# Performance work log

Hardware: AMD Instinct MI355X
Metric: run time of the kernel (lower is better)

The kernel has to match this reference:

```python
import jax, jax.numpy as jnp
import numpy as np

NUM_HEADS = 16


def setup_inputs() -> dict:
    key = jax.random.key(0)
    ks = jax.random.split(key, 9)
    B, N, D = 2, 2048, 1024
    w = 0.02
    return {
        "x": jax.random.normal(ks[0], (B, N, D), dtype=jnp.float32),
        "wq": jax.random.normal(ks[1], (D, D), dtype=jnp.float32) * w,
        "bq": jax.random.normal(ks[2], (D,), dtype=jnp.float32) * w,
        "wk": jax.random.normal(ks[3], (D, D), dtype=jnp.float32) * w,
        "bk": jax.random.normal(ks[4], (D,), dtype=jnp.float32) * w,
        "wv": jax.random.normal(ks[5], (D, D), dtype=jnp.float32) * w,
        "bv": jax.random.normal(ks[6], (D,), dtype=jnp.float32) * w,
        "wo": jax.random.normal(ks[7], (D, D), dtype=jnp.float32) * w,
        "bo": jax.random.normal(ks[8], (D,), dtype=jnp.float32) * w,
    }


def _heads(t, B, N, H, hd):
    # (B, N, D) -> (B, H, N, hd)
    return t.reshape(B, N, H, hd).transpose(0, 2, 1, 3)


def reference(x, wq, bq, wk, bk, wv, bv, wo, bo):
    B, N, D = x.shape
    H = NUM_HEADS
    hd = D // H
    q = _heads(x @ wq.T + bq, B, N, H, hd)
    k = _heads(x @ wk.T + bk, B, N, H, hd)
    v = _heads(x @ wv.T + bv, B, N, H, hd)
    # pairwise L2 distances via GEMM expansion: ||q-k||^2 = |q|^2 + |k|^2 - 2 q.k
    q2 = jnp.sum(q * q, axis=-1)                      # (B, H, N)
    k2 = jnp.sum(k * k, axis=-1)                      # (B, H, N)
    qk = jnp.einsum('bhid,bhjd->bhij', q, k)          # (B, H, N, N)
    d2 = jnp.maximum(q2[..., :, None] + k2[..., None, :] - 2.0 * qk, 1e-12)
    attn = jax.nn.softmax(-jnp.sqrt(d2), axis=-1)     # (B, H, N, N)
    out = jnp.einsum('bhij,bhjd->bhid', attn, v)      # (B, H, N, hd)
    out = out.transpose(0, 2, 1, 3).reshape(B, N, D)
    return out @ wo.T + bo
```

## Files before the change

### kernel.cpp

```cpp
#include <hip/hip_runtime.h>


typedef __attribute__((ext_vector_type(8))) short sh8;
typedef __attribute__((ext_vector_type(4))) short sh4;
typedef __attribute__((ext_vector_type(4))) float f4;

#define QK_SCALE 1.44269504f
#define D2_CLAMP 2.0814e-12f

__device__ __forceinline__ float bf2f(short s) {
  union { unsigned u; float f; } c;
  c.u = ((unsigned)(unsigned short)s) << 16;
  return c.f;
}
__device__ __forceinline__ short f2bf(float f) {
  union { float f; unsigned u; } c;
  c.f = f;
  return (short)((c.u + 0x8000u) >> 16);
}
__device__ __forceinline__ sh8 pack8(f4 a, f4 b) {
  sh8 r;
  r[0] = f2bf(a[0]); r[1] = f2bf(a[1]); r[2] = f2bf(a[2]); r[3] = f2bf(a[3]);
  r[4] = f2bf(b[0]); r[5] = f2bf(b[1]); r[6] = f2bf(b[2]); r[7] = f2bf(b[3]);
  return r;
}
__device__ __forceinline__ float exp2neg(float x) {
  return __builtin_amdgcn_exp2f(-x);
}

#define GLDS16(g, l)                                                      \
  __builtin_amdgcn_global_load_lds(                                       \
      (__attribute__((address_space(1))) void*)(void*)(g),                \
      (__attribute__((address_space(3))) void*)(void*)(l), 16, 0, 0)

__global__ __launch_bounds__(256) void cvt_bf16(const float* __restrict__ src,
                                                short* __restrict__ dst, int n) {
  const int i = (blockIdx.x * 256 + threadIdx.x) * 8;
  if (i < n)
    *(sh8*)(dst + i) = pack8(*(const f4*)(src + i), *(const f4*)(src + i + 4));
}

__global__ __launch_bounds__(256) void cvt_w4(
    const float* __restrict__ wq, const float* __restrict__ wk,
    const float* __restrict__ wv, const float* __restrict__ wo,
    short* __restrict__ dst) {
  const float* srcs[4] = {wq, wk, wv, wo};
  const float* s = srcs[blockIdx.y];
  short* d = dst + (size_t)blockIdx.y * 1048576;
  const int i = (blockIdx.x * 256 + threadIdx.x) * 8;
  *(sh8*)(d + i) = pack8(*(const f4*)(s + i), *(const f4*)(s + i + 4));
}

__global__ __launch_bounds__(256) void gemm_qkvp(
    const float* __restrict__ X, const float* __restrict__ Wq,
    const float* __restrict__ Bq, const float* __restrict__ Wk,
    const float* __restrict__ Bk, const float* __restrict__ Wv,
    const float* __restrict__ Bv, short* __restrict__ Qp,
    short* __restrict__ Kp, short* __restrict__ Vtp, int w0, int nblkP) {
  __shared__ short As[128 * 32];
  __shared__ short Bs[128 * 32];
  const int t = threadIdx.x;
  const int wave = t >> 6;
  const int lane = t & 63;
  const int l15 = lane & 15;
  const int quad = lane >> 4;
  const int m0 = blockIdx.y * 128;
  const int which = blockIdx.x / nblkP;
  const int n0l = (blockIdx.x % nblkP) * 128;
  const int wrow0 = w0 + n0l;
  const float* W = (which == 0) ? Wq : ((which == 1) ? Wk : Wv);
  const float* Bias = (which == 0) ? Bq : ((which == 1) ? Bk : Bv);
  const float qkscl = (which == 2) ? 1.0f : QK_SCALE;
  const int wm = (wave & 1) * 64;
  const int wn = (wave >> 1) * 64;

  f4 acc[4][4];
#pragma unroll
  for (int i = 0; i < 4; ++i)
#pragma unroll
    for (int j = 0; j < 4; ++j) acc[i][j] = (f4){0.f, 0.f, 0.f, 0.f};

  const float* ag = X + (size_t)(m0 + (t >> 2)) * 1024 + (t & 3) * 8;
  const float* bg = W + (size_t)(wrow0 + (t >> 2)) * 1024 + (t & 3) * 8;

  for (int kt = 0; kt < 1024; kt += 32) {
    const sh8 a0 = pack8(*(const f4*)(ag + kt), *(const f4*)(ag + kt + 4));
    const sh8 a1 =
        pack8(*(const f4*)(ag + 65536 + kt), *(const f4*)(ag + 65536 + kt + 4));
    const sh8 b0 = pack8(*(const f4*)(bg + kt), *(const f4*)(bg + kt + 4));
    const sh8 b1 =
        pack8(*(const f4*)(bg + 65536 + kt), *(const f4*)(bg + 65536 + kt + 4));
    __syncthreads();
    *(sh8*)(As + t * 8) = a0;
    *(sh8*)(As + 2048 + t * 8) = a1;
    *(sh8*)(Bs + t * 8) = b0;
    *(sh8*)(Bs + 2048 + t * 8) = b1;
    __syncthreads();
    sh8 af[4], bf[4];
#pragma unroll
    for (int i = 0; i < 4; ++i) {
      af[i] = *(const sh8*)(As + (wm + i * 16 + l15) * 32 + quad * 8);
      bf[i] = *(const sh8*)(Bs + (wn + i * 16 + l15) * 32 + quad * 8);
    }
#pragma unroll
    for (int i = 0; i < 4; ++i)
#pragma unroll
      for (int j = 0; j < 4; ++j)
        acc[i][j] =
            __builtin_amdgcn_mfma_f32_16x16x32_bf16(af[i], bf[j], acc[i][j], 0, 0, 0);
  }

#pragma unroll
  for (int j = 0; j < 4; ++j) {
    const int ngl = n0l + wn + j * 16 + l15;
    const float bias = Bias[w0 + ngl];
    const int hl = ngl >> 6;
    const int d = ngl & 63;
#pragma unroll
    for (int i = 0; i < 4; ++i) {
#pragma unroll
      for (int r = 0; r < 4; ++r) {
        const int m = m0 + wm + i * 16 + quad * 4 + r;
        const int slot = (m >> 11) * 16 + hl;
        const int mm = m & 2047;
        const short o = f2bf((acc[i][j][r] + bias) * qkscl);
        if (which == 0)
          Qp[((size_t)slot * 2048 + mm) * 64 + d] = o;
        else if (which == 1)
          Kp[((size_t)slot * 2048 + mm) * 64 + d] = o;
        else
          Vtp[((size_t)slot * 64 + d) * 2048 + mm] = o;
      }
    }
  }
}

__global__ __launch_bounds__(256) void gemm_qkv_bf(
    const short* __restrict__ X, const short* __restrict__ Wq,
    const float* __restrict__ Bq, const short* __restrict__ Wk,
    const float* __restrict__ Bk, const short* __restrict__ Wv,
    const float* __restrict__ Bv, short* __restrict__ Qp,
    short* __restrict__ Kp, short* __restrict__ Vtp) {
  __shared__ short As[128 * 32];
  __shared__ short Bs[128 * 32];
  const int t = threadIdx.x;
  const int wave = t >> 6;
  const int lane = t & 63;
  const int l15 = lane & 15;
  const int quad = lane >> 4;
  const int m0 = blockIdx.y * 128;
  const int which = blockIdx.x >> 3;
  const int n0l = (blockIdx.x & 7) * 128;
  const short* W = (which == 0) ? Wq : ((which == 1) ? Wk : Wv);
  const float* Bias = (which == 0) ? Bq : ((which == 1) ? Bk : Bv);
  const float qkscl = (which == 2) ? 1.0f : QK_SCALE;
  const int wm = (wave & 1) * 64;
  const int wn = (wave >> 1) * 64;

  f4 acc[4][4];
#pragma unroll
  for (int i = 0; i < 4; ++i)
#pragma unroll
    for (int j = 0; j < 4; ++j) acc[i][j] = (f4){0.f, 0.f, 0.f, 0.f};

  const short* ag = X + (size_t)(m0 + (t >> 2)) * 1024 + (t & 3) * 8;
  const short* bg = W + (size_t)(n0l + (t >> 2)) * 1024 + (t & 3) * 8;
  short* al = As + wave * 512;
  short* bl = Bs + wave * 512;

  for (int kt = 0; kt < 1024; kt += 32) {
    __syncthreads();
    GLDS16(ag + kt, al);
    GLDS16(ag + 65536 + kt, al + 2048);
    GLDS16(bg + kt, bl);
    GLDS16(bg + 65536 + kt, bl + 2048);
    __syncthreads();
    sh8 af[4], bf[4];
#pragma unroll
    for (int i = 0; i < 4; ++i) {
      af[i] = *(const sh8*)(As + (wm + i * 16 + l15) * 32 + quad * 8);
      bf[i] = *(const sh8*)(Bs + (wn + i * 16 + l15) * 32 + quad * 8);
    }
#pragma unroll
    for (int i = 0; i < 4; ++i)
#pragma unroll
      for (int j = 0; j < 4; ++j)
        acc[i][j] =
            __builtin_amdgcn_mfma_f32_16x16x32_bf16(af[i], bf[j], acc[i][j], 0, 0, 0);
  }

#pragma unroll
  for (int j = 0; j < 4; ++j) {
    const int ngl = n0l + wn + j * 16 + l15;
    const float bias = Bias[ngl];
    const int hl = ngl >> 6;
    const int d = ngl & 63;
#pragma unroll
    for (int i = 0; i < 4; ++i) {
#pragma unroll
      for (int r = 0; r < 4; ++r) {
        const int m = m0 + wm + i * 16 + quad * 4 + r;
        const int slot = (m >> 11) * 16 + hl;
        const int mm = m & 2047;
        const short o = f2bf((acc[i][j][r] + bias) * qkscl);
        if (which == 0)
          Qp[((size_t)slot * 2048 + mm) * 64 + d] = o;
        else if (which == 1)
          Kp[((size_t)slot * 2048 + mm) * 64 + d] = o;
        else
          Vtp[((size_t)slot * 64 + d) * 2048 + mm] = o;
      }
    }
  }
}

__global__ __launch_bounds__(256) void sumsq(const short* __restrict__ Qp,
                                             const short* __restrict__ Kp,
                                             float* __restrict__ q2a,
                                             float* __restrict__ k2a, int R) {
  const int tid = blockIdx.x * 256 + threadIdx.x;
  const bool isQ = tid < R;
  const int r = isQ ? tid : tid - R;
  const short* p = (isQ ? Qp : Kp) + (size_t)r * 64;
  float s = 0.f;
#pragma unroll
  for (int i = 0; i < 8; ++i) {
    sh8 v = *(const sh8*)(p + i * 8);
#pragma unroll
    for (int j = 0; j < 8; ++j) {
      float f = bf2f(v[j]);
      s = fmaf(f, f, s);
    }
  }
  (isQ ? q2a : k2a)[r] = s;
}

__global__ __launch_bounds__(256, 4) void attn9(
    const short* __restrict__ Qp, const short* __restrict__ Kp,
    const short* __restrict__ Vtp, const float* __restrict__ q2a,
    const float* __restrict__ k2a, short* __restrict__ attH) {
  __shared__ short Ks[128 * 64];
  __shared__ short Vs[64 * 128];
  const int t = threadIdx.x;
  const int wave = t >> 6;
  const int lane = t & 63;
  const int l15 = lane & 15;
  const int quad = lane >> 4;
  const int id = blockIdx.x;
  const int qt = (id >> 3) & 31;
  const int hb_ = (id & 7) * 4 + (id >> 8);
  const int hy = hb_ & 15;
  const int bz = hb_ >> 4;
  const size_t hb = (size_t)hb_;
  const size_t base = hb * 2048;
  const int qrow = qt * 64 + wave * 16 + l15;

  const short* qp = Qp + (base + qrow) * 64 + quad * 8;
  const sh8 qf0 = *(const sh8*)qp;
  const sh8 qf1 = *(const sh8*)(qp + 32);
  const float q2 = q2a[base + qrow];

  float l_run = 0.f;
  f4 o0 = (f4){0.f, 0.f, 0.f, 0.f}, o1 = o0, o2 = o0, o3 = o0;

  const float* k2p = k2a + base + quad * 4;

  const int kr = t >> 3, kc = t & 7;
  const int vr = t >> 4, vc = t & 15;
  const short* kg0 = Kp + (base + kr) * 64 + kc * 8;
  const short* vg0 = Vtp + (hb * 64 + vr) * 2048 + vc * 8;
  const int kidx = kr * 64 + ((kc ^ (kr & 7)) * 8);
  const int vidx = vr * 128 + ((vc ^ (vr & 7)) * 8);

  sh8 kp0 = *(const sh8*)kg0;
  sh8 kp1 = *(const sh8*)(kg0 + 32 * 64);
  sh8 kp2 = *(const sh8*)(kg0 + 64 * 64);
  sh8 kp3 = *(const sh8*)(kg0 + 96 * 64);
  sh8 vp0 = *(const sh8*)vg0;
  sh8 vp1 = *(const sh8*)(vg0 + 16 * 2048);
  sh8 vp2 = *(const sh8*)(vg0 + 32 * 2048);
  sh8 vp3 = *(const sh8*)(vg0 + 48 * 2048);

  for (int k0 = 0; k0 < 2048; k0 += 128) {
    __syncthreads();
    *(sh8*)(Ks + kidx) = kp0;
    *(sh8*)(Ks + 32 * 64 + kidx) = kp1;
    *(sh8*)(Ks + 64 * 64 + kidx) = kp2;
    *(sh8*)(Ks + 96 * 64 + kidx) = kp3;
    *(sh8*)(Vs + vidx) = vp0;
    *(sh8*)(Vs + 16 * 128 + vidx) = vp1;
    *(sh8*)(Vs + 32 * 128 + vidx) = vp2;
    *(sh8*)(Vs + 48 * 128 + vidx) = vp3;
    __syncthreads();
    if (k0 + 128 < 2048) {
      const short* kg = kg0 + (size_t)(k0 + 128) * 64;
      kp0 = *(const sh8*)kg;
      kp1 = *(const sh8*)(kg + 32 * 64);
      kp2 = *(const sh8*)(kg + 64 * 64);
      kp3 = *(const sh8*)(kg + 96 * 64);
      const short* vg = vg0 + k0 + 128;
      vp0 = *(const sh8*)vg;
      vp1 = *(const sh8*)(vg + 16 * 2048);
      vp2 = *(const sh8*)(vg + 32 * 2048);
      vp3 = *(const sh8*)(vg + 48 * 2048);
    }

#pragma unroll
    for (int sub = 0; sub < 8; ++sub) {
      const int j = sub * 16;
      const int krow = j + l15;
      const int kcs = (quad ^ (krow & 7)) * 8;
      const sh8 kf0 = *(const sh8*)(Ks + krow * 64 + kcs);
      const sh8 kf1 = *(const sh8*)(Ks + krow * 64 + (kcs ^ 32));
      f4 st = (f4){0.f, 0.f, 0.f, 0.f};
      st = __builtin_amdgcn_mfma_f32_16x16x32_bf16(kf0, qf0, st, 0, 0, 0);
      st = __builtin_amdgcn_mfma_f32_16x16x32_bf16(kf1, qf1, st, 0, 0, 0);
      const f4 k2v = *(const f4*)(k2p + k0 + j);
      float p[4];
#pragma unroll
      for (int r = 0; r < 4; ++r) {
        const float d2 = fmaf(-2.f, st[r], q2 + k2v[r]);
        p[r] = exp2neg(__builtin_amdgcn_sqrtf(fabsf(d2)));
      }
      l_run += (p[0] + p[1]) + (p[2] + p[3]);
      sh4 pf;
#pragma unroll
      for (int r = 0; r < 4; ++r) pf[r] = f2bf(p[r]);
      const int vcol = ((sub * 2 + (quad >> 1)) ^ (l15 & 7)) * 8 + (quad & 1) * 4;
      const sh4 vf0 = *(const sh4*)(Vs + l15 * 128 + vcol);
      const sh4 vf1 = *(const sh4*)(Vs + (l15 + 16) * 128 + vcol);
      const sh4 vf2 = *(const sh4*)(Vs + (l15 + 32) * 128 + vcol);
      const sh4 vf3 = *(const sh4*)(Vs + (l15 + 48) * 128 + vcol);
      o0 = __builtin_amdgcn_mfma_f32_16x16x16bf16_1k(pf, vf0, o0, 0, 0, 0);
      o1 = __builtin_amdgcn_mfma_f32_16x16x16bf16_1k(pf, vf1, o1, 0, 0, 0);
      o2 = __builtin_amdgcn_mfma_f32_16x16x16bf16_1k(pf, vf2, o2, 0, 0, 0);
      o3 = __builtin_amdgcn_mfma_f32_16x16x16bf16_1k(pf, vf3, o3, 0, 0, 0);
    }
  }

  l_run += __shfl_xor(l_run, 16);
  l_run += __shfl_xor(l_run, 32);
  const float il0 = 1.f / __shfl(l_run, quad * 4 + 0);
  const float il1 = 1.f / __shfl(l_run, quad * 4 + 1);
  const float il2 = 1.f / __shfl(l_run, quad * 4 + 2);
  const float il3 = 1.f / __shfl(l_run, quad * 4 + 3);

  const int rowbase = qt * 64 + wave * 16 + quad * 4;
  const f4* oc[4] = {&o0, &o1, &o2, &o3};
  const float il[4] = {il0, il1, il2, il3};
  const size_t off0 = ((size_t)bz * 2048 + rowbase) * 1024 + hy * 64 + l15;
#pragma unroll
  for (int c = 0; c < 4; ++c)
#pragma unroll
    for (int r = 0; r < 4; ++r)
      attH[off0 + (size_t)r * 1024 + c * 16] = f2bf((*oc[c])[r] * il[r]);
}

__global__ __launch_bounds__(256) void attn_c(
    const short* __restrict__ Qp, const short* __restrict__ Kp,
    const short* __restrict__ Vtp, const float* __restrict__ q2a,
    const float* __restrict__ k2a, float* __restrict__ attF, int col0) {
  const int t = threadIdx.x;
  const int wave = t >> 6;
  const int lane = t & 63;
  const int l15 = lane & 15;
  const int quad = lane >> 4;
  const int hy = blockIdx.y;
  const int qt = blockIdx.x;
  const size_t base = (size_t)hy * 2048;
  const int qrow = qt * 64 + wave * 16 + l15;

  const short* qp = Qp + (base + qrow) * 64 + quad * 8;
  const sh8 qf0 = *(const sh8*)qp;
  const sh8 qf1 = *(const sh8*)(qp + 32);
  const float q2 = q2a[base + qrow];

  float l_run = 0.f;
  f4 o0 = (f4){0.f, 0.f, 0.f, 0.f}, o1 = o0, o2 = o0, o3 = o0;

  const short* kbase = Kp + (base + l15) * 64 + quad * 8;
  const float* k2p = k2a + base + quad * 4;
  const short* vbase = Vtp + ((size_t)hy * 64 + l15) * 2048 + quad * 4;

  for (int j = 0; j < 2048; j += 16) {
    const sh8 kf0 = *(const sh8*)(kbase + (size_t)j * 64);
    const sh8 kf1 = *(const sh8*)(kbase + (size_t)j * 64 + 32);
    f4 st = (f4){0.f, 0.f, 0.f, 0.f};
    st = __builtin_amdgcn_mfma_f32_16x16x32_bf16(kf0, qf0, st, 0, 0, 0);
    st = __builtin_amdgcn_mfma_f32_16x16x32_bf16(kf1, qf1, st, 0, 0, 0);
    const f4 k2v = *(const f4*)(k2p + j);
    float p[4];
#pragma unroll
    for (int r = 0; r < 4; ++r) {
      const float d2 = fmaxf(fmaf(-2.f, st[r], q2 + k2v[r]), D2_CLAMP);
      p[r] = exp2neg(__builtin_amdgcn_sqrtf(d2));
    }
    l_run += (p[0] + p[1]) + (p[2] + p[3]);
    sh4 pf;
#pragma unroll
    for (int r = 0; r < 4; ++r) pf[r] = f2bf(p[r]);
    const sh4 vf0 = *(const sh4*)(vbase + j);
    const sh4 vf1 = *(const sh4*)(vbase + 16 * 2048 + j);
    const sh4 vf2 = *(const sh4*)(vbase + 32 * 2048 + j);
    const sh4 vf3 = *(const sh4*)(vbase + 48 * 2048 + j);
    o0 = __builtin_amdgcn_mfma_f32_16x16x16bf16_1k(pf, vf0, o0, 0, 0, 0);
    o1 = __builtin_amdgcn_mfma_f32_16x16x16bf16_1k(pf, vf1, o1, 0, 0, 0);
    o2 = __builtin_amdgcn_mfma_f32_16x16x16bf16_1k(pf, vf2, o2, 0, 0, 0);
    o3 = __builtin_amdgcn_mfma_f32_16x16x16bf16_1k(pf, vf3, o3, 0, 0, 0);
  }

  l_run += __shfl_xor(l_run, 16);
  l_run += __shfl_xor(l_run, 32);
  const float il0 = 1.f / __shfl(l_run, quad * 4 + 0);
  const float il1 = 1.f / __shfl(l_run, quad * 4 + 1);
  const float il2 = 1.f / __shfl(l_run, quad * 4 + 2);
  const float il3 = 1.f / __shfl(l_run, quad * 4 + 3);

  const int rowbase = qt * 64 + wave * 16 + quad * 4;
  const f4* oc[4] = {&o0, &o1, &o2, &o3};
  const float il[4] = {il0, il1, il2, il3};
  const size_t off0 = (size_t)rowbase * 1024 + col0 + hy * 64 + l15;
#pragma unroll
  for (int c = 0; c < 4; ++c)
#pragma unroll
    for (int r = 0; r < 4; ++r)
      attF[off0 + (size_t)r * 1024 + c * 16] = (*oc[c])[r] * il[r];
}

__global__ __launch_bounds__(256) void gemm_out_bf64(
    const short* __restrict__ A, const short* __restrict__ W,
    const float* __restrict__ Bias, float* __restrict__ Out) {
  __shared__ short As[64 * 32];
  __shared__ short Bs[128 * 32];
  const int t = threadIdx.x;
  const int wave = t >> 6;
  const int lane = t & 63;
  const int l15 = lane & 15;
  const int quad = lane >> 4;
  const int m0 = blockIdx.y * 64;
  const int n0 = blockIdx.x * 128;
  const int wm = (wave & 1) * 32;
  const int wn = (wave >> 1) * 64;

  f4 acc[2][4];
#pragma unroll
  for (int i = 0; i < 2; ++i)
#pragma unroll
    for (int j = 0; j < 4; ++j) acc[i][j] = (f4){0.f, 0.f, 0.f, 0.f};

  const short* ag = A + (size_t)(m0 + (t >> 2)) * 1024 + (t & 3) * 8;
  const short* bg = W + (size_t)(n0 + (t >> 2)) * 1024 + (t & 3) * 8;
  short* al = As + wave * 512;
  short* bl = Bs + wave * 512;

  for (int kt = 0; kt < 1024; kt += 32) {
    __syncthreads();
    GLDS16(ag + kt, al);
    GLDS16(bg + kt, bl);
    GLDS16(bg + 65536 + kt, bl + 2048);
    __syncthreads();
    sh8 af[2], bf[4];
#pragma unroll
    for (int i = 0; i < 2; ++i)
      af[i] = *(const sh8*)(As + (wm + i * 16 + l15) * 32 + quad * 8);
#pragma unroll
    for (int j = 0; j < 4; ++j)
      bf[j] = *(const sh8*)(Bs + (wn + j * 16 + l15) * 32 + quad * 8);
#pragma unroll
    for (int i = 0; i < 2; ++i)
#pragma unroll
      for (int j = 0; j < 4; ++j)
        acc[i][j] =
            __builtin_amdgcn_mfma_f32_16x16x32_bf16(af[i], bf[j], acc[i][j], 0, 0, 0);
  }

#pragma unroll
  for (int j = 0; j < 4; ++j) {
    const int n = n0 + wn + j * 16 + l15;
    const float bias = Bias[n];
#pragma unroll
    for (int i = 0; i < 2; ++i) {
#pragma unroll
      for (int r = 0; r < 4; ++r) {
        const int m = m0 + wm + i * 16 + quad * 4 + r;
        Out[(size_t)m * 1024 + n] = acc[i][j][r] + bias;
      }
    }
  }
}

__global__ __launch_bounds__(256) void gemm_out_ws64(
    const short* __restrict__ A, const float* __restrict__ W,
    const float* __restrict__ Bias, float* __restrict__ Out) {
  __shared__ short As[64 * 32];
  __shared__ short Bs[128 * 32];
  const int t = threadIdx.x;
  const int wave = t >> 6;
  const int lane = t & 63;
  const int l15 = lane & 15;
  const int quad = lane >> 4;
  const int m0 = blockIdx.y * 64;
  const int n0 = blockIdx.x * 128;
  const int wm = (wave & 1) * 32;
  const int wn = (wave >> 1) * 64;

  f4 acc[2][4];
#pragma unroll
  for (int i = 0; i < 2; ++i)
#pragma unroll
    for (int j = 0; j < 4; ++j) acc[i][j] = (f4){0.f, 0.f, 0.f, 0.f};

  const short* ag = A + (size_t)(m0 + (t >> 2)) * 1024 + (t & 3) * 8;
  const float* bg = W + (size_t)(n0 + (t >> 2)) * 1024 + (t & 3) * 8;
  short* al = As + wave * 512;

  for (int kt = 0; kt < 1024; kt += 32) {
    const sh8 b0 = pack8(*(const f4*)(bg + kt), *(const f4*)(bg + kt + 4));
    const sh8 b1 =
        pack8(*(const f4*)(bg + 65536 + kt), *(const f4*)(bg + 65536 + kt + 4));
    __syncthreads();
    GLDS16(ag + kt, al);
    *(sh8*)(Bs + t * 8) = b0;
    *(sh8*)(Bs + 2048 + t * 8) = b1;
    __syncthreads();
    sh8 af[2], bf[4];
#pragma unroll
    for (int i = 0; i < 2; ++i)
      af[i] = *(const sh8*)(As + (wm + i * 16 + l15) * 32 + quad * 8);
#pragma unroll
    for (int j = 0; j < 4; ++j)
      bf[j] = *(const sh8*)(Bs + (wn + j * 16 + l15) * 32 + quad * 8);
#pragma unroll
    for (int i = 0; i < 2; ++i)
#pragma unroll
      for (int j = 0; j < 4; ++j)
        acc[i][j] =
            __builtin_amdgcn_mfma_f32_16x16x32_bf16(af[i], bf[j], acc[i][j], 0, 0, 0);
  }

#pragma unroll
  for (int j = 0; j < 4; ++j) {
    const int n = n0 + wn + j * 16 + l15;
    const float bias = Bias[n];
#pragma unroll
    for (int i = 0; i < 2; ++i) {
#pragma unroll
      for (int r = 0; r < 4; ++r) {
        const int m = m0 + wm + i * 16 + quad * 4 + r;
        Out[(size_t)m * 1024 + n] = acc[i][j][r] + bias;
      }
    }
  }
}

__global__ __launch_bounds__(256) void outproj_inplace(
    float* __restrict__ AO, const float* __restrict__ W,
    const float* __restrict__ Bias) {
  __shared__ short attS[16 * 264];
  const int t = threadIdx.x;
  const int wave = t >> 6;
  const int lane = t & 63;
  const int l15 = lane & 15;
  const int quad = lane >> 4;
  const int m0 = blockIdx.x * 16;
  const int n0w = wave * 256;

  f4 acc[16];
#pragma unroll
  for (int i = 0; i < 16; ++i) acc[i] = (f4){0.f, 0.f, 0.f, 0.f};

  for (int kc = 0; kc < 4; ++kc) {
    __syncthreads();
#pragma unroll
    for (int i = 0; i < 2; ++i) {
      const int e = i * 2048 + t * 8;
      const int row = e >> 8;
      const int col = e & 255;
      const float* src = AO + (size_t)(m0 + row) * 1024 + kc * 256 + col;
      *(sh8*)(attS + row * 264 + col) =
          pack8(*(const f4*)src, *(const f4*)(src + 4));
    }
    __syncthreads();
    for (int ktl = 0; ktl < 256; ktl += 32) {
      const sh8 af = *(const sh8*)(attS + l15 * 264 + ktl + quad * 8);
      const int kt = kc * 256 + ktl;
#pragma unroll
      for (int nf = 0; nf < 16; ++nf) {
        const float* wp = W + (size_t)(n0w + nf * 16 + l15) * 1024 + kt + quad * 8;
        const sh8 bf = pack8(*(const f4*)wp, *(const f4*)(wp + 4));
        acc[nf] = __builtin_amdgcn_mfma_f32_16x16x32_bf16(af, bf, acc[nf], 0, 0, 0);
      }
    }
  }
  __syncthreads();

#pragma unroll
  for (int nf = 0; nf < 16; ++nf) {
    const int n = n0w + nf * 16 + l15;
    const float bias = Bias[n];
#pragma unroll
    for (int r = 0; r < 4; ++r) {
      const int m = m0 + quad * 4 + r;
      AO[(size_t)m * 1024 + n] = acc[nf][r] + bias;
    }
  }
}

extern "C" void kernel_launch(void* const* d_in, const int* in_sizes, int n_in,
                              void* d_out, int out_size, void* d_ws,
                              size_t ws_size, hipStream_t stream) {
  const float* x = (const float*)d_in[0];
  const float* wq = (const float*)d_in[1];
  const float* bq = (const float*)d_in[2];
  const float* wk = (const float*)d_in[3];
  const float* bk = (const float*)d_in[4];
  const float* wv = (const float*)d_in[5];
  const float* bv = (const float*)d_in[6];
  const float* wo = (const float*)d_in[7];
  const float* bo = (const float*)d_in[8];
  float* out = (float*)d_out;

  const size_t NEED_A2 = 50855936ULL;
  const size_t NEED_A = 34078720ULL;

  if (ws_size >= NEED_A) {
    short* Qp = (short*)d_ws;
    short* Kp = Qp + 4194304;
    short* Vtp = Kp + 4194304;
    short* attAll = Vtp + 4194304;
    float* q2 = (float*)(attAll + 4194304);
    float* k2 = q2 + 65536;

    if (ws_size >= NEED_A2) {
      short* Xb = (short*)(k2 + 65536);
      short* Wqb = Xb + 4194304;
      cvt_bf16<<<2048, 256, 0, stream>>>(x, Xb, 4194304);
      cvt_w4<<<dim3(512, 4), 256, 0, stream>>>(wq, wk, wv, wo, Wqb);
      gemm_qkv_bf<<<dim3(24, 32), 256, 0, stream>>>(
          Xb, Wqb, bq, Wqb + 1048576, bk, Wqb + 2097152, bv, Qp, Kp, Vtp);
      sumsq<<<512, 256, 0, stream>>>(Qp, Kp, q2, k2, 65536);
      attn9<<<1024, 256, 0, stream>>>(Qp, Kp, Vtp, q2, k2, attAll);
      gemm_out_bf64<<<dim3(8, 64), 256, 0, stream>>>(attAll, Wqb + 3145728,
                                                     bo, out);
    } else {
      gemm_qkvp<<<dim3(24, 32), 256, 0, stream>>>(x, wq, bq, wk, bk, wv, bv,
                                                  Qp, Kp, Vtp, 0, 8);
      sumsq<<<512, 256, 0, stream>>>(Qp, Kp, q2, k2, 65536);
      attn9<<<1024, 256, 0, stream>>>(Qp, Kp, Vtp, q2, k2, attAll);
      gemm_out_ws64<<<dim3(8, 64), 256, 0, stream>>>(attAll, wo, bo, out);
    }
  } else {
    int G = 16;
    while (G > 2 && (size_t)G * 802816ULL > ws_size) G >>= 1;
    short* Qp = (short*)d_ws;
    short* Kp = Qp + (size_t)G * 131072;
    short* Vtp = Kp + (size_t)G * 131072;
    float* q2 = (float*)(Vtp + (size_t)G * 131072);
    float* k2 = q2 + (size_t)G * 2048;

    const int groups = 16 / G;
    for (int b = 0; b < 2; ++b) {
      const float* xb = x + (size_t)b * 2097152;
      float* attB = out + (size_t)b * 2097152;
      for (int g = 0; g < groups; ++g) {
        gemm_qkvp<<<dim3(3 * (G / 2), 16), 256, 0, stream>>>(
            xb, wq, bq, wk, bk, wv, bv, Qp, Kp, Vtp, g * G * 64, G / 2);
        sumsq<<<16 * G, 256, 0, stream>>>(Qp, Kp, q2, k2, G * 2048);
        attn_c<<<dim3(32, G), 256, 0, stream>>>(Qp, Kp, Vtp, q2, k2, attB,
                                                g * G * 64);
      }
    }
    outproj_inplace<<<256, 256, 0, stream>>>(out, wo, bo);
  }
}
```

Measured before the change: 236.5 us.

## Read K and V fragments directly from global memory in attention kernel

Drops the LDS staging of K and V tiles, their software prefetch into registers and the two block barriers per tile. Each wave now loads its MFMA fragments straight from global memory (through L1/L2), one 16-key slice at a time. This removes barrier and LDS traffic, but each of the four waves in a block now fetches the same K/V data separately and global-load latency is no longer hidden by explicit prefetch.

```diff
diff --git a/kernel.cpp b/kernel.cpp
--- a/kernel.cpp
+++ b/kernel.cpp
@@ -235,12 +235,10 @@
   (isQ ? q2a : k2a)[r] = s;
 }
 
-__global__ __launch_bounds__(256, 4) void attn9(
+__global__ __launch_bounds__(256, 4) void attn_g(
     const short* __restrict__ Qp, const short* __restrict__ Kp,
     const short* __restrict__ Vtp, const float* __restrict__ q2a,
     const float* __restrict__ k2a, short* __restrict__ attH) {
-  __shared__ short Ks[128 * 64];
-  __shared__ short Vs[64 * 128];
   const int t = threadIdx.x;
   const int wave = t >> 6;
   const int lane = t & 63;
@@ -251,8 +249,7 @@
   const int hb_ = (id & 7) * 4 + (id >> 8);
   const int hy = hb_ & 15;
   const int bz = hb_ >> 4;
-  const size_t hb = (size_t)hb_;
-  const size_t base = hb * 2048;
+  const size_t base = (size_t)hb_ * 2048;
   const int qrow = qt * 64 + wave * 16 + l15;
 
   const short* qp = Qp + (base + qrow) * 64 + quad * 8;
@@ -263,79 +260,35 @@
   float l_run = 0.f;
   f4 o0 = (f4){0.f, 0.f, 0.f, 0.f}, o1 = o0, o2 = o0, o3 = o0;
 
+  const short* kbase = Kp + (base + l15) * 64 + quad * 8;
   const float* k2p = k2a + base + quad * 4;
-
-  const int kr = t >> 3, kc = t & 7;
-  const int vr = t >> 4, vc = t & 15;
-  const short* kg0 = Kp + (base + kr) * 64 + kc * 8;
-  const short* vg0 = Vtp + (hb * 64 + vr) * 2048 + vc * 8;
-  const int kidx = kr * 64 + ((kc ^ (kr & 7)) * 8);
-  const int vidx = vr * 128 + ((vc ^ (vr & 7)) * 8);
-
-  sh8 kp0 = *(const sh8*)kg0;
-  sh8 kp1 = *(const sh8*)(kg0 + 32 * 64);
-  sh8 kp2 = *(const sh8*)(kg0 + 64 * 64);
-  sh8 kp3 = *(const sh8*)(kg0 + 96 * 64);
-  sh8 vp0 = *(const sh8*)vg0;
-  sh8 vp1 = *(const sh8*)(vg0 + 16 * 2048);
-  sh8 vp2 = *(const sh8*)(vg0 + 32 * 2048);
-  sh8 vp3 = *(const sh8*)(vg0 + 48 * 2048);
-
-  for (int k0 = 0; k0 < 2048; k0 += 128) {
-    __syncthreads();
-    *(sh8*)(Ks + kidx) = kp0;
-    *(sh8*)(Ks + 32 * 64 + kidx) = kp1;
-    *(sh8*)(Ks + 64 * 64 + kidx) = kp2;
-    *(sh8*)(Ks + 96 * 64 + kidx) = kp3;
-    *(sh8*)(Vs + vidx) = vp0;
-    *(sh8*)(Vs + 16 * 128 + vidx) = vp1;
-    *(sh8*)(Vs + 32 * 128 + vidx) = vp2;
-    *(sh8*)(Vs + 48 * 128 + vidx) = vp3;
-    __syncthreads();
-    if (k0 + 128 < 2048) {
-      const short* kg = kg0 + (size_t)(k0 + 128) * 64;
-      kp0 = *(const sh8*)kg;
-      kp1 = *(const sh8*)(kg + 32 * 64);
-      kp2 = *(const sh8*)(kg + 64 * 64);
-      kp3 = *(const sh8*)(kg + 96 * 64);
-      const short* vg = vg0 + k0 + 128;
-      vp0 = *(const sh8*)vg;
-      vp1 = *(const sh8*)(vg + 16 * 2048);
-      vp2 = *(const sh8*)(vg + 32 * 2048);
-      vp3 = *(const sh8*)(vg + 48 * 2048);
-    }
-
-#pragma unroll
-    for (int sub = 0; sub < 8; ++sub) {
-      const int j = sub * 16;
-      const int krow = j + l15;
-      const int kcs = (quad ^ (krow & 7)) * 8;
-      const sh8 kf0 = *(const sh8*)(Ks + krow * 64 + kcs);
-      const sh8 kf1 = *(const sh8*)(Ks + krow * 64 + (kcs ^ 32));
-      f4 st = (f4){0.f, 0.f, 0.f, 0.f};
-      st = __builtin_amdgcn_mfma_f32_16x16x32_bf16(kf0, qf0, st, 0, 0, 0);
-      st = __builtin_amdgcn_mfma_f32_16x16x32_bf16(kf1, qf1, st, 0, 0, 0);
-      const f4 k2v = *(const f4*)(k2p + k0 + j);
-      float p[4];
-#pragma unroll
-      for (int r = 0; r < 4; ++r) {
-        const float d2 = fmaf(-2.f, st[r], q2 + k2v[r]);
-        p[r] = exp2neg(__builtin_amdgcn_sqrtf(fabsf(d2)));
-      }
-      l_run += (p[0] + p[1]) + (p[2] + p[3]);
-      sh4 pf;
-#pragma unroll
-      for (int r = 0; r < 4; ++r) pf[r] = f2bf(p[r]);
-      const int vcol = ((sub * 2 + (quad >> 1)) ^ (l15 & 7)) * 8 + (quad & 1) * 4;
-      const sh4 vf0 = *(const sh4*)(Vs + l15 * 128 + vcol);
-      const sh4 vf1 = *(const sh4*)(Vs + (l15 + 16) * 128 + vcol);
-      const sh4 vf2 = *(const sh4*)(Vs + (l15 + 32) * 128 + vcol);
-      const sh4 vf3 = *(const sh4*)(Vs + (l15 + 48) * 128 + vcol);
-      o0 = __builtin_amdgcn_mfma_f32_16x16x16bf16_1k(pf, vf0, o0, 0, 0, 0);
-      o1 = __builtin_amdgcn_mfma_f32_16x16x16bf16_1k(pf, vf1, o1, 0, 0, 0);
-      o2 = __builtin_amdgcn_mfma_f32_16x16x16bf16_1k(pf, vf2, o2, 0, 0, 0);
-      o3 = __builtin_amdgcn_mfma_f32_16x16x16bf16_1k(pf, vf3, o3, 0, 0, 0);
-    }
+  const short* vbase = Vtp + ((size_t)hb_ * 64 + l15) * 2048 + quad * 4;
+
+  for (int j = 0; j < 2048; j += 16) {
+    const sh8 kf0 = *(const sh8*)(kbase + (size_t)j * 64);
+    const sh8 kf1 = *(const sh8*)(kbase + (size_t)j * 64 + 32);
+    f4 st = (f4){0.f, 0.f, 0.f, 0.f};
+    st = __builtin_amdgcn_mfma_f32_16x16x32_bf16(kf0, qf0, st, 0, 0, 0);
+    st = __builtin_amdgcn_mfma_f32_16x16x32_bf16(kf1, qf1, st, 0, 0, 0);
+    const f4 k2v = *(const f4*)(k2p + j);
+    float p[4];
+#pragma unroll
+    for (int r = 0; r < 4; ++r) {
+      const float d2 = fmaf(-2.f, st[r], q2 + k2v[r]);
+      p[r] = exp2neg(__builtin_amdgcn_sqrtf(fabsf(d2)));
+    }
+    l_run += (p[0] + p[1]) + (p[2] + p[3]);
+    sh4 pf;
+#pragma unroll
+    for (int r = 0; r < 4; ++r) pf[r] = f2bf(p[r]);
+    const sh4 vf0 = *(const sh4*)(vbase + j);
+    const sh4 vf1 = *(const sh4*)(vbase + 16 * 2048 + j);
+    const sh4 vf2 = *(const sh4*)(vbase + 32 * 2048 + j);
+    const sh4 vf3 = *(const sh4*)(vbase + 48 * 2048 + j);
+    o0 = __builtin_amdgcn_mfma_f32_16x16x16bf16_1k(pf, vf0, o0, 0, 0, 0);
+    o1 = __builtin_amdgcn_mfma_f32_16x16x16bf16_1k(pf, vf1, o1, 0, 0, 0);
+    o2 = __builtin_amdgcn_mfma_f32_16x16x16bf16_1k(pf, vf2, o2, 0, 0, 0);
+    o3 = __builtin_amdgcn_mfma_f32_16x16x16bf16_1k(pf, vf3, o3, 0, 0, 0);
   }
 
   l_run += __shfl_xor(l_run, 16);
@@ -639,14 +592,14 @@
       gemm_qkv_bf<<<dim3(24, 32), 256, 0, stream>>>(
           Xb, Wqb, bq, Wqb + 1048576, bk, Wqb + 2097152, bv, Qp, Kp, Vtp);
       sumsq<<<512, 256, 0, stream>>>(Qp, Kp, q2, k2, 65536);
-      attn9<<<1024, 256, 0, stream>>>(Qp, Kp, Vtp, q2, k2, attAll);
+      attn_g<<<1024, 256, 0, stream>>>(Qp, Kp, Vtp, q2, k2, attAll);
       gemm_out_bf64<<<dim3(8, 64), 256, 0, stream>>>(attAll, Wqb + 3145728,
                                                      bo, out);
     } else {
       gemm_qkvp<<<dim3(24, 32), 256, 0, stream>>>(x, wq, bq, wk, bk, wv, bv,
                                                   Qp, Kp, Vtp, 0, 8);
       sumsq<<<512, 256, 0, stream>>>(Qp, Kp, q2, k2, 65536);
-      attn9<<<1024, 256, 0, stream>>>(Qp, Kp, Vtp, q2, k2, attAll);
+      attn_g<<<1024, 256, 0, stream>>>(Qp, Kp, Vtp, q2, k2, attAll);
       gemm_out_ws64<<<dim3(8, 64), 256, 0, stream>>>(attAll, wo, bo, out);
     }
   } else {
```

Result: slower. 505.5 us (+113.8%).
